# Kernel optimization log

Measured on AMD Instinct MI355X. Metric: run time of the kernel, lower is better.

## Reference

```python
import jax, jax.numpy as jnp
import numpy as np

Q_UPPER = 64  # number of quantization bins for upper-layer distributions
CLIP_LO, CLIP_HI = 1e-15, 1e15


def setup_inputs() -> dict:
    key = jax.random.key(0)
    k = jax.random.split(key, 6)
    B, NU, NL, QU, QL = 256, 64, 64, Q_UPPER, 64
    w_init = 0.1
    P = jax.random.uniform(k[0], (B, NL, QL), dtype=jnp.float32)
    weight = jax.random.uniform(k[1], (NU, NL), minval=-w_init, maxval=w_init, dtype=jnp.float32)
    bias_abs = jax.random.uniform(k[2], (NU, 1), minval=-w_init, maxval=w_init, dtype=jnp.float32)
    bias_q = jax.random.uniform(k[3], (NU, 1), minval=-w_init, maxval=w_init, dtype=jnp.float32)
    lambda_abs = jax.random.uniform(k[4], (NU, 1), minval=0.0, maxval=1.0, dtype=jnp.float32)
    lambda_q = jax.random.uniform(k[5], (NU, 1), minval=0.0, maxval=1.0, dtype=jnp.float32)
    return {"P": P, "weight": weight, "bias_abs": bias_abs, "bias_q": bias_q,
            "lambda_abs": lambda_abs, "lambda_q": lambda_q}


def reference(P, weight, bias_abs, bias_q, lambda_abs, lambda_q):
    # P: [B, n_lower, q_lower]; weight: [n_upper, n_lower]; biases/lambdas: [n_upper, 1]
    QU = Q_UPPER
    QL = P.shape[2]
    s1 = jnp.arange(QU, dtype=P.dtype) / QU          # upper bin centers
    s0 = jnp.arange(QL, dtype=P.dtype) / QL          # lower bin centers
    diff2 = (s0[None, :] - s1[:, None]) ** 2          # [QU, QL]
    # D = exp(-diff2); T = D**weight = exp(-weight * diff2), permuted to [NU, NL, QU, QL]
    T = jnp.exp(-weight[:, :, None, None] * diff2[None, None, :, :])
    # batched GEMV over q_lower: Pw[i,j,k,l] = sum_m T[j,k,l,m] * P[i,k,m]
    Pw = jnp.einsum('jklm,ikm->ijkl', T, P)           # [B, NU, NL, QU]
    logPw = jnp.log(jnp.clip(Pw, CLIP_LO, CLIP_HI))
    logsum = jnp.sum(logPw, axis=2)                   # [B, NU, QU]
    sq = jnp.arange(QU, dtype=P.dtype)[None, :] / QU  # [1, QU]
    exponent_B = (-bias_q * (sq - lambda_q) ** 2
                  - bias_abs * jnp.abs(sq - lambda_abs))  # [NU, QU]
    logsumB = logsum + exponent_B[None, :, :]
    return jax.nn.softmax(logsumB, axis=2)            # [B, NU, QU]
```

## Files before the change

### kernel.cpp

```cpp
#include <hip/hip_runtime.h>


#define NUP 64
#define NLOW 64
#define QUP 64
#define QLOW 64

__global__ __launch_bounds__(512, 4)
void drn_kernel(const float* __restrict__ P,
                const float* __restrict__ weight,
                const float* __restrict__ bias_abs,
                const float* __restrict__ bias_q,
                const float* __restrict__ lambda_abs,
                const float* __restrict__ lambda_q,
                float* __restrict__ out)
{
    __shared__ float  lds_mom[NLOW * 12];
    __shared__ float4 lds_n[NLOW * QUP];

    const int i    = blockIdx.x >> 1;
    const int jh   = blockIdx.x & 1;
    const int tid  = threadIdx.x;
    const int lane = tid & 63;
    const int wv   = __builtin_amdgcn_readfirstlane(tid >> 6);

    {
        const int kk = lane >> 3;
        const int mc = lane & 7;
        const int k  = wv * 8 + kk;
        const float* Pr = P + ((size_t)i * NLOW + k) * QLOW + mc * 8;
        const float4 pa = *reinterpret_cast<const float4*>(Pr);
        const float4 pb = *reinterpret_cast<const float4*>(Pr + 4);

        float t0 = 0.f, t1 = 0.f, t2 = 0.f, t3 = 0.f, t4 = 0.f,
              t5 = 0.f, t6 = 0.f, t7 = 0.f, t8 = 0.f;
        const float s0 = (float)(mc * 8) * 0.015625f;
#define ACCM(PV, S) { float f = (PV); const float s_ = (S); \
        t0 += f; f *= s_; t1 += f; f *= s_; t2 += f; f *= s_; t3 += f; f *= s_; \
        t4 += f; f *= s_; t5 += f; f *= s_; t6 += f; f *= s_; t7 += f; f *= s_; t8 += f; }
        ACCM(pa.x, s0);
        ACCM(pa.y, s0 + 0.015625f);
        ACCM(pa.z, s0 + 0.03125f);
        ACCM(pa.w, s0 + 0.046875f);
        ACCM(pb.x, s0 + 0.0625f);
        ACCM(pb.y, s0 + 0.078125f);
        ACCM(pb.z, s0 + 0.09375f);
        ACCM(pb.w, s0 + 0.109375f);
#undef ACCM
#define RED9(OFF) { t0 += __shfl_xor(t0, OFF, 64); t1 += __shfl_xor(t1, OFF, 64); \
        t2 += __shfl_xor(t2, OFF, 64); t3 += __shfl_xor(t3, OFF, 64); \
        t4 += __shfl_xor(t4, OFF, 64); t5 += __shfl_xor(t5, OFF, 64); \
        t6 += __shfl_xor(t6, OFF, 64); t7 += __shfl_xor(t7, OFF, 64); \
        t8 += __shfl_xor(t8, OFF, 64); }
        RED9(1) RED9(2) RED9(4)
#undef RED9
        if (mc == 0) {
            float* mp = &lds_mom[k * 12];
            *reinterpret_cast<float4*>(mp)     = make_float4(t0, t1, t2, t3);
            *reinterpret_cast<float4*>(mp + 4) = make_float4(t4, t5, t6, t7);
            mp[8] = t8;
        }
    }
    __syncthreads();

    const float s1l = (float)lane * 0.015625f;
    {
        const float z  = -s1l;
        const float z2 = z * z, z3 = z2 * z, z4 = z2 * z2;
        const float z5 = z4 * z, z6 = z4 * z2, z7 = z6 * z, z8 = z4 * z4;
        const float c10 = z2,                c11 = 2.f * z;
        const float c20 = 0.5f * z4,         c21 = 2.f * z3,          c22 = 3.f * z2,
                    c23 = 2.f * z;
        const float c30 = z6 * (1.f / 6.f),  c31 = z5,                c32 = 2.5f * z4,
                    c33 = (10.f / 3.f) * z3, c34 = 2.5f * z2,         c35 = z;
        const float c40 = z8 * (1.f / 24.f), c41 = z7 * (1.f / 3.f),  c42 = (7.f / 6.f) * z6,
                    c43 = (7.f / 3.f) * z5,  c44 = (35.f / 12.f) * z4, c45 = (7.f / 3.f) * z3,
                    c46 = (7.f / 6.f) * z2,  c47 = z * (1.f / 3.f);

#pragma unroll
        for (int kk = 0; kk < 8; ++kk) {
            const int k = wv * 8 + kk;
            const float4 q0 = *reinterpret_cast<const float4*>(&lds_mom[k * 12]);
            const float4 q1 = *reinterpret_cast<const float4*>(&lds_mom[k * 12 + 4]);
            const float  q8 = lds_mom[k * 12 + 8];

            const float inv = 1.0f / q0.x;
            const float m1 = fmaf(c10, q0.x, fmaf(c11, q0.y, q0.z));
            const float m2 = fmaf(c20, q0.x, fmaf(c21, q0.y, fmaf(c22, q0.z,
                             fmaf(c23, q0.w, 0.5f * q1.x))));
            const float m3 = fmaf(c30, q0.x, fmaf(c31, q0.y, fmaf(c32, q0.z,
                             fmaf(c33, q0.w, fmaf(c34, q1.x, fmaf(c35, q1.y,
                             (1.f / 6.f) * q1.z))))));
            const float m4 = fmaf(c40, q0.x, fmaf(c41, q0.y, fmaf(c42, q0.z,
                             fmaf(c43, q0.w, fmaf(c44, q1.x, fmaf(c45, q1.y,
                             fmaf(c46, q1.z, fmaf(c47, q1.w, (1.f / 24.f) * q8))))))));

            lds_n[k * QUP + lane] = make_float4(m1 * inv, m2 * inv, m3 * inv, m4 * inv);
        }
    }
    __syncthreads();

    const float* __restrict__ w0r = weight + (size_t)(jh * 32 + wv * 4 + 0) * NLOW;
    const float* __restrict__ w1r = weight + (size_t)(jh * 32 + wv * 4 + 1) * NLOW;
    const float* __restrict__ w2r = weight + (size_t)(jh * 32 + wv * 4 + 2) * NLOW;
    const float* __restrict__ w3r = weight + (size_t)(jh * 32 + wv * 4 + 3) * NLOW;

    float pr0 = 1.f, pr1 = 1.f, pr2 = 1.f, pr3 = 1.f;
    for (int k8 = 0; k8 < 8; ++k8) {
        float w0[8], w1[8], w2[8], w3[8];
#pragma unroll
        for (int kk = 0; kk < 8; ++kk) {
            w0[kk] = w0r[k8 * 8 + kk];
            w1[kk] = w1r[k8 * 8 + kk];
            w2[kk] = w2r[k8 * 8 + kk];
            w3[kk] = w3r[k8 * 8 + kk];
        }
#pragma unroll
        for (int kk = 0; kk < 8; ++kk) {
            const float4 n = lds_n[(k8 * 8 + kk) * QUP + lane];
#define STEPJ(W, PR) { const float w_ = (W); \
            float t = fmaf(-w_, n.w, n.z); \
            t = fmaf(-w_, t, n.y); t = fmaf(-w_, t, n.x); \
            PR *= fmaf(-w_, t, 1.0f); }
            STEPJ(w0[kk], pr0)
            STEPJ(w1[kk], pr1)
            STEPJ(w2[kk], pr2)
            STEPJ(w3[kk], pr3)
#undef STEPJ
        }
    }

    const float LOG2E = 1.4426950408889634f;
    const float acc0 = __log2f(pr0);
    const float acc1 = __log2f(pr1);
    const float acc2 = __log2f(pr2);
    const float acc3 = __log2f(pr3);
    auto finish = [&](float a, int jj) {
        const int j = jh * 32 + wv * 4 + jj;
        const float dq = s1l - lambda_q[j];
        float y = fmaf(-bias_q[j] * LOG2E, dq * dq, a);
        y = fmaf(-bias_abs[j] * LOG2E, fabsf(s1l - lambda_abs[j]), y);
        float mx = y;
#pragma unroll
        for (int off = 32; off >= 1; off >>= 1)
            mx = fmaxf(mx, __shfl_xor(mx, off, 64));
        const float e = exp2f(y - mx);
        float s = e;
#pragma unroll
        for (int off = 32; off >= 1; off >>= 1)
            s += __shfl_xor(s, off, 64);
        out[((size_t)i * NUP + j) * QUP + lane] = e / s;
    };
    finish(acc0, 0);
    finish(acc1, 1);
    finish(acc2, 2);
    finish(acc3, 3);
}

extern "C" void kernel_launch(void* const* d_in, const int* in_sizes, int n_in,
                              void* d_out, int out_size, void* d_ws, size_t ws_size,
                              hipStream_t stream) {
    const float* P          = (const float*)d_in[0];
    const float* weight     = (const float*)d_in[1];
    const float* bias_abs   = (const float*)d_in[2];
    const float* bias_q     = (const float*)d_in[3];
    const float* lambda_abs = (const float*)d_in[4];
    const float* lambda_q   = (const float*)d_in[5];
    (void)in_sizes; (void)n_in; (void)out_size; (void)d_ws; (void)ws_size;

    drn_kernel<<<dim3(512), dim3(512), 0, stream>>>(
        P, weight, bias_abs, bias_q, lambda_abs, lambda_q, (float*)d_out);
}
```

Baseline: 76.21 us.

## Process all upper units per block and broadcast weights via readlane

Each block now handles one batch row and all 64 upper units (8 per wave) instead of splitting the units over two blocks. This halves the grid and removes the duplicated moment and polynomial-coefficient computation per batch row. Weights are loaded once per lane into registers and broadcast with readlane, replacing the repeated scalar global loads. The trade-off is fewer blocks (256 on a large GPU) and higher register pressure, with launch bounds relaxed to 2 blocks per CU to allow it.

```diff
diff --git a/kernel.cpp b/kernel.cpp
--- a/kernel.cpp
+++ b/kernel.cpp
@@ -6,7 +6,7 @@
 #define QUP 64
 #define QLOW 64
 
-__global__ __launch_bounds__(512, 4)
+__global__ __launch_bounds__(512, 2)
 void drn_kernel(const float* __restrict__ P,
                 const float* __restrict__ weight,
                 const float* __restrict__ bias_abs,
@@ -18,11 +18,15 @@
     __shared__ float  lds_mom[NLOW * 12];
     __shared__ float4 lds_n[NLOW * QUP];
 
-    const int i    = blockIdx.x >> 1;
-    const int jh   = blockIdx.x & 1;
+    const int i    = blockIdx.x;
     const int tid  = threadIdx.x;
     const int lane = tid & 63;
     const int wv   = __builtin_amdgcn_readfirstlane(tid >> 6);
+
+    float wreg[8];
+#pragma unroll
+    for (int jj = 0; jj < 8; ++jj)
+        wreg[jj] = weight[(size_t)(wv * 8 + jj) * NLOW + lane];
 
     {
         const int kk = lane >> 3;
@@ -100,45 +104,34 @@
     }
     __syncthreads();
 
-    const float* __restrict__ w0r = weight + (size_t)(jh * 32 + wv * 4 + 0) * NLOW;
-    const float* __restrict__ w1r = weight + (size_t)(jh * 32 + wv * 4 + 1) * NLOW;
-    const float* __restrict__ w2r = weight + (size_t)(jh * 32 + wv * 4 + 2) * NLOW;
-    const float* __restrict__ w3r = weight + (size_t)(jh * 32 + wv * 4 + 3) * NLOW;
+    float pr[8];
+#pragma unroll
+    for (int jj = 0; jj < 8; ++jj) pr[jj] = 1.0f;
 
-    float pr0 = 1.f, pr1 = 1.f, pr2 = 1.f, pr3 = 1.f;
     for (int k8 = 0; k8 < 8; ++k8) {
-        float w0[8], w1[8], w2[8], w3[8];
 #pragma unroll
         for (int kk = 0; kk < 8; ++kk) {
-            w0[kk] = w0r[k8 * 8 + kk];
-            w1[kk] = w1r[k8 * 8 + kk];
-            w2[kk] = w2r[k8 * 8 + kk];
-            w3[kk] = w3r[k8 * 8 + kk];
-        }
+            const int k = k8 * 8 + kk;
+            const float4 n = lds_n[k * QUP + lane];
 #pragma unroll
-        for (int kk = 0; kk < 8; ++kk) {
-            const float4 n = lds_n[(k8 * 8 + kk) * QUP + lane];
-#define STEPJ(W, PR) { const float w_ = (W); \
-            float t = fmaf(-w_, n.w, n.z); \
-            t = fmaf(-w_, t, n.y); t = fmaf(-w_, t, n.x); \
-            PR *= fmaf(-w_, t, 1.0f); }
-            STEPJ(w0[kk], pr0)
-            STEPJ(w1[kk], pr1)
-            STEPJ(w2[kk], pr2)
-            STEPJ(w3[kk], pr3)
-#undef STEPJ
+            for (int jj = 0; jj < 8; ++jj) {
+                const float w_ = __int_as_float(
+                    __builtin_amdgcn_readlane(__float_as_int(wreg[jj]), k));
+                float t = fmaf(-w_, n.w, n.z);
+                t = fmaf(-w_, t, n.y);
+                t = fmaf(-w_, t, n.x);
+                pr[jj] *= fmaf(-w_, t, 1.0f);
+            }
         }
     }
 
     const float LOG2E = 1.4426950408889634f;
-    const float acc0 = __log2f(pr0);
-    const float acc1 = __log2f(pr1);
-    const float acc2 = __log2f(pr2);
-    const float acc3 = __log2f(pr3);
-    auto finish = [&](float a, int jj) {
-        const int j = jh * 32 + wv * 4 + jj;
+#pragma unroll
+    for (int jj = 0; jj < 8; ++jj) {
+        const int j = wv * 8 + jj;
         const float dq = s1l - lambda_q[j];
-        float y = fmaf(-bias_q[j] * LOG2E, dq * dq, a);
+        float y = __log2f(pr[jj]);
+        y = fmaf(-bias_q[j] * LOG2E, dq * dq, y);
         y = fmaf(-bias_abs[j] * LOG2E, fabsf(s1l - lambda_abs[j]), y);
         float mx = y;
 #pragma unroll
@@ -150,11 +143,7 @@
         for (int off = 32; off >= 1; off >>= 1)
             s += __shfl_xor(s, off, 64);
         out[((size_t)i * NUP + j) * QUP + lane] = e / s;
-    };
-    finish(acc0, 0);
-    finish(acc1, 1);
-    finish(acc2, 2);
-    finish(acc3, 3);
+    }
 }
 
 extern "C" void kernel_launch(void* const* d_in, const int* in_sizes, int n_in,
@@ -168,6 +157,6 @@
     const float* lambda_q   = (const float*)d_in[5];
     (void)in_sizes; (void)n_in; (void)out_size; (void)d_ws; (void)ws_size;
 
-    drn_kernel<<<dim3(512), dim3(512), 0, stream>>>(
+    drn_kernel<<<dim3(256), dim3(512), 0, stream>>>(
         P, weight, bias_abs, bias_q, lambda_abs, lambda_q, (float*)d_out);
 }
```

Result: slower. 78.81 us (+3.4%).
